# Kernel tuning notes

Hardware: AMD Instinct MI355X
Metric: run time of the kernel (lower is better)

## Reference

```python
import jax, jax.numpy as jnp
import numpy as np

D_MODEL = 512
NHEAD = 8
D_K = D_MODEL // NHEAD
SCALE = float(np.sqrt(D_K))


def setup_inputs() -> dict:
    key = jax.random.key(0)
    ks = jax.random.split(key, 11)
    B, S = 2, 4096
    std = 1.0 / np.sqrt(D_MODEL)
    inp = {
        'q': jax.random.normal(ks[0], (B, S, D_MODEL), jnp.float32),
        'k': jax.random.normal(ks[1], (B, S, D_MODEL), jnp.float32),
        'v': jax.random.normal(ks[2], (B, S, D_MODEL), jnp.float32),
        'w_q': jax.random.normal(ks[3], (D_MODEL, D_MODEL), jnp.float32) * std,
        'b_q': jax.random.normal(ks[4], (D_MODEL,), jnp.float32) * std,
        'w_k': jax.random.normal(ks[5], (D_MODEL, D_MODEL), jnp.float32) * std,
        'b_k': jax.random.normal(ks[6], (D_MODEL,), jnp.float32) * std,
        'w_v': jax.random.normal(ks[7], (D_MODEL, D_MODEL), jnp.float32) * std,
        'b_v': jax.random.normal(ks[8], (D_MODEL,), jnp.float32) * std,
        'w_o': jax.random.normal(ks[9], (D_MODEL, D_MODEL), jnp.float32) * std,
        'b_o': jax.random.normal(ks[10], (D_MODEL,), jnp.float32) * std,
    }
    return inp


def reference(q, k, v, w_q, b_q, w_k, b_k, w_v, b_v, w_o, b_o):
    B, S, _ = q.shape
    # torch Linear: y = x @ W.T + b
    def proj(x, W, b):
        y = x @ W.T + b
        return y.reshape(B, -1, NHEAD, D_K).transpose(0, 2, 1, 3)  # [B,H,S,Dk]
    qh = proj(q, w_q, b_q)
    kh = proj(k, w_k, b_k)
    vh = proj(v, w_v, b_v)
    scores = jnp.einsum('bhsd,bhtd->bhst', qh, kh) / SCALE  # [B,H,S,S]
    attn = jax.nn.softmax(scores, axis=-1)
    out = jnp.einsum('bhst,bhtd->bhsd', attn, vh)  # [B,H,S,Dk]
    out = out.transpose(0, 2, 1, 3).reshape(B, S, D_MODEL)
    return out @ w_o.T + b_o
```

## Files before the change

### kernel.cpp

```cpp
#include <hip/hip_runtime.h>
#include <stdint.h>

#define DM 512
#define S_LEN 4096
#define NH 8
#define DK 64

typedef __attribute__((ext_vector_type(8))) short bf16x8;
typedef __attribute__((ext_vector_type(4))) float f32x4;

#define QSCALE 0.18033688011112042f
#define NEGBIAS -17.312340490667562f

__device__ inline ushort f2bf(float f) {
  union { float f; uint32_t u; } v; v.f = f;
  uint32_t r = v.u + 0x7fff + ((v.u >> 16) & 1);
  return (ushort)(r >> 16);
}
__device__ inline uint32_t fu(float f) {
  union { float f; uint32_t u; } v; v.f = f; return v.u;
}
__device__ inline uint32_t pktrunc(float lo, float hi) {
  return __builtin_amdgcn_perm(fu(hi), fu(lo), 0x07060302);
}

__device__ inline void async_cp16(const ushort* g, ushort* l) {
  __builtin_amdgcn_global_load_lds((const __attribute__((address_space(1))) void*)g,
                                   (__attribute__((address_space(3))) void*)l, 16, 0, 0);
}

__global__ __launch_bounds__(256) void cvt_w(const float4* __restrict__ s0, ushort* __restrict__ d0,
                                             const float4* __restrict__ s1, ushort* __restrict__ d1,
                                             const float4* __restrict__ s2, ushort* __restrict__ d2,
                                             const float4* __restrict__ s3, ushort* __restrict__ d3) {
  int i = blockIdx.x * 256 + threadIdx.x;
  {
    float4 v = s0[i];
    ushort4 o = {f2bf(v.x), f2bf(v.y), f2bf(v.z), f2bf(v.w)};
    *(ushort4*)&d0[i * 4] = o;
  }
  {
    float4 v = s1[i];
    ushort4 o = {f2bf(v.x), f2bf(v.y), f2bf(v.z), f2bf(v.w)};
    *(ushort4*)&d1[i * 4] = o;
  }
  {
    float4 v = s2[i];
    ushort4 o = {f2bf(v.x), f2bf(v.y), f2bf(v.z), f2bf(v.w)};
    *(ushort4*)&d2[i * 4] = o;
  }
  {
    float4 v = s3[i];
    ushort4 o = {f2bf(v.x), f2bf(v.y), f2bf(v.z), f2bf(v.w)};
    *(ushort4*)&d3[i * 4] = o;
  }
}

__global__ __launch_bounds__(256) void gemm_proj(
    const float* __restrict__ q, const float* __restrict__ k, const float* __restrict__ v,
    const ushort* __restrict__ wq, const ushort* __restrict__ wk, const ushort* __restrict__ wv,
    const float* __restrict__ bq, const float* __restrict__ bk, const float* __restrict__ bv,
    ushort* __restrict__ Qh, ushort* __restrict__ Kh, ushort* __restrict__ VhT) {
  const float* A; const ushort* Bt; const float* bias; float cs;
  if (blockIdx.z == 0)      { A = q; Bt = wq; bias = bq; cs = QSCALE; }
  else if (blockIdx.z == 1) { A = k; Bt = wk; bias = bk; cs = 1.0f; }
  else                      { A = v; Bt = wv; bias = bv; cs = 1.0f; }

  __shared__ ushort As[64 * 32];
  __shared__ ushort Bs[128 * 32];
  const int tid = threadIdx.x;
  const int w = tid >> 6, lane = tid & 63;
  const int quad = lane >> 4, l16 = lane & 15;
  const int wm = w >> 1, wn = w & 1;
  const int m0 = blockIdx.y * 64, n0 = blockIdx.x * 128;
  const f32x4 zero4 = {0.f, 0.f, 0.f, 0.f};

  f32x4 acc[2][4];
  #pragma unroll
  for (int i = 0; i < 2; i++)
    #pragma unroll
    for (int j = 0; j < 4; j++) acc[i][j] = zero4;

  for (int kb = 0; kb < 16; kb++) {
    const int k0 = kb * 32;
    #pragma unroll
    for (int r = 0; r < 2; r++) {
      int idx = r * 256 + tid;
      async_cp16(&Bt[(size_t)(n0 + (idx >> 2)) * DM + k0 + (idx & 3) * 8], &Bs[idx * 8]);
    }
    {
      int row = tid >> 2, col = (tid & 3) * 8;
      const float* src = &A[(size_t)(m0 + row) * DM + k0 + col];
      float4 a0 = *(const float4*)src;
      float4 a1 = *(const float4*)(src + 4);
      uint2 w0 = {pktrunc(a0.x, a0.y), pktrunc(a0.z, a0.w)};
      uint2 w1 = {pktrunc(a1.x, a1.y), pktrunc(a1.z, a1.w)};
      *(uint2*)&As[row * 32 + col] = w0;
      *(uint2*)&As[row * 32 + col + 4] = w1;
    }
    __syncthreads();
    bf16x8 af[2], bfr[4];
    #pragma unroll
    for (int i = 0; i < 2; i++)
      af[i] = *(const bf16x8*)&As[(wm * 32 + i * 16 + l16) * 32 + quad * 8];
    #pragma unroll
    for (int j = 0; j < 4; j++)
      bfr[j] = *(const bf16x8*)&Bs[(wn * 64 + j * 16 + l16) * 32 + quad * 8];
    #pragma unroll
    for (int i = 0; i < 2; i++)
      #pragma unroll
      for (int j = 0; j < 4; j++)
        acc[i][j] = __builtin_amdgcn_mfma_f32_16x16x32_bf16(af[i], bfr[j], acc[i][j], 0, 0, 0);
    __syncthreads();
  }

  if (blockIdx.z != 2) {
    ushort* C = (blockIdx.z == 0) ? Qh : Kh;
    #pragma unroll
    for (int j = 0; j < 4; j++) {
      int col_g = n0 + wn * 64 + j * 16 + l16;
      float bv = bias[col_g];
      int h = col_g >> 6, d = col_g & 63;
      #pragma unroll
      for (int i = 0; i < 2; i++) {
        #pragma unroll
        for (int r = 0; r < 4; r++) {
          int row_g = m0 + wm * 32 + i * 16 + quad * 4 + r;
          int b = row_g >> 12, s = row_g & 4095;
          C[(((size_t)(b * NH + h) << 12) + s) * DK + d] = f2bf((acc[i][j][r] + bv) * cs);
        }
      }
    }
  } else {
    #pragma unroll
    for (int j = 0; j < 4; j++) {
      int col_g = n0 + wn * 64 + j * 16 + l16;
      float bv = bias[col_g];
      int h = col_g >> 6, d = col_g & 63;
      #pragma unroll
      for (int i = 0; i < 2; i++) {
        int row0 = m0 + wm * 32 + i * 16 + quad * 4;
        int b = row0 >> 12, s0 = row0 & 4095;
        ushort4 pk = {f2bf(acc[i][j][0] + bv), f2bf(acc[i][j][1] + bv),
                      f2bf(acc[i][j][2] + bv), f2bf(acc[i][j][3] + bv)};
        *(ushort4*)&VhT[((size_t)(b * NH + h) * DK + d) * S_LEN + s0] = pk;
      }
    }
  }
}

__global__ __launch_bounds__(256) void gemm_out(const ushort* __restrict__ A,
                                                const ushort* __restrict__ Bt,
                                                const float* __restrict__ bias,
                                                float* __restrict__ C) {
  __shared__ ushort As[64 * 32];
  __shared__ ushort Bs[128 * 32];
  const int tid = threadIdx.x;
  const int w = tid >> 6, lane = tid & 63;
  const int quad = lane >> 4, l16 = lane & 15;
  const int wm = w >> 1, wn = w & 1;
  const int m0 = blockIdx.y * 64, n0 = blockIdx.x * 128;
  const f32x4 zero4 = {0.f, 0.f, 0.f, 0.f};

  f32x4 acc[2][4];
  #pragma unroll
  for (int i = 0; i < 2; i++)
    #pragma unroll
    for (int j = 0; j < 4; j++) acc[i][j] = zero4;

  for (int kb = 0; kb < 16; kb++) {
    const int k0 = kb * 32;
    async_cp16(&A[(size_t)(m0 + (tid >> 2)) * DM + k0 + (tid & 3) * 8], &As[tid * 8]);
    #pragma unroll
    for (int r = 0; r < 2; r++) {
      int idx = r * 256 + tid;
      async_cp16(&Bt[(size_t)(n0 + (idx >> 2)) * DM + k0 + (idx & 3) * 8], &Bs[idx * 8]);
    }
    __syncthreads();
    bf16x8 af[2], bfr[4];
    #pragma unroll
    for (int i = 0; i < 2; i++)
      af[i] = *(const bf16x8*)&As[(wm * 32 + i * 16 + l16) * 32 + quad * 8];
    #pragma unroll
    for (int j = 0; j < 4; j++)
      bfr[j] = *(const bf16x8*)&Bs[(wn * 64 + j * 16 + l16) * 32 + quad * 8];
    #pragma unroll
    for (int i = 0; i < 2; i++)
      #pragma unroll
      for (int j = 0; j < 4; j++)
        acc[i][j] = __builtin_amdgcn_mfma_f32_16x16x32_bf16(af[i], bfr[j], acc[i][j], 0, 0, 0);
    __syncthreads();
  }

  #pragma unroll
  for (int j = 0; j < 4; j++) {
    int col_g = n0 + wn * 64 + j * 16 + l16;
    float bv = bias[col_g];
    #pragma unroll
    for (int i = 0; i < 2; i++) {
      #pragma unroll
      for (int r = 0; r < 4; r++) {
        int row_g = m0 + wm * 32 + i * 16 + quad * 4 + r;
        C[(size_t)row_g * DM + col_g] = acc[i][j][r] + bv;
      }
    }
  }
}

__global__ __launch_bounds__(256, 2) void attn(const ushort* __restrict__ Qh,
                                               const ushort* __restrict__ Kh,
                                               const ushort* __restrict__ VhT,
                                               ushort* __restrict__ O) {
  __shared__ ushort Ks[128 * 72];
  __shared__ ushort Vt[64 * 136];
  const int tid = threadIdx.x;
  const int w = tid >> 6, lane = tid & 63;
  const int quad = lane >> 4, l16 = lane & 15;
  const int bh = blockIdx.x;
  const int q0 = blockIdx.y * 128 + w * 32;
  const size_t base = (size_t)bh * S_LEN * DK;
  const f32x4 zero4 = {0.f, 0.f, 0.f, 0.f};
  const f32x4 negb = {NEGBIAS, NEGBIAS, NEGBIAS, NEGBIAS};
  const short one_bf = (short)0x3F80;
  const bf16x8 ones = {one_bf, one_bf, one_bf, one_bf, one_bf, one_bf, one_bf, one_bf};

  bf16x8 qf[2][2];
  #pragma unroll
  for (int i = 0; i < 2; i++)
    #pragma unroll
    for (int c = 0; c < 2; c++)
      qf[i][c] = *(const bf16x8*)&Qh[base + (size_t)(q0 + i * 16 + l16) * DK + c * 32 + quad * 8];

  f32x4 o[2][4];
  f32x4 l_acc[2];
  #pragma unroll
  for (int i = 0; i < 2; i++) {
    l_acc[i] = zero4;
    #pragma unroll
    for (int n = 0; n < 4; n++) o[i][n] = zero4;
  }

  for (int it = 0; it < 32; it++) {
    const int t0 = it * 128;
    #pragma unroll
    for (int r = 0; r < 4; r++) {
      int idx = r * 256 + tid;
      int row = idx >> 3, col = (idx & 7) * 8;
      *(uint4*)&Ks[row * 72 + col] = *(const uint4*)&Kh[base + (size_t)(t0 + row) * DK + col];
    }
    #pragma unroll
    for (int r = 0; r < 4; r++) {
      int idx = r * 256 + tid;
      int row = idx >> 4, colc = (idx & 15) * 8;
      uint4 vv = *(const uint4*)&VhT[base + (size_t)row * S_LEN + t0 + colc];
      int bpos = (colc & ~31) + ((colc >> 2) & 3) * 8 + ((colc >> 4) & 1) * 4;
      uint2 lo = {vv.x, vv.y}, hi = {vv.z, vv.w};
      *(uint2*)&Vt[row * 136 + bpos] = lo;
      *(uint2*)&Vt[row * 136 + bpos + 8] = hi;
    }
    __syncthreads();

    #pragma unroll
    for (int half = 0; half < 2; half++) {
      bf16x8 kf[4][2];
      #pragma unroll
      for (int s = 0; s < 4; s++) {
        int sub = half * 4 + s;
        kf[s][0] = *(const bf16x8*)&Ks[(sub * 16 + l16) * 72 + quad * 8];
        kf[s][1] = *(const bf16x8*)&Ks[(sub * 16 + l16) * 72 + 32 + quad * 8];
      }
      f32x4 sc[2][4];
      #pragma unroll
      for (int i = 0; i < 2; i++)
        #pragma unroll
        for (int s = 0; s < 4; s++) {
          f32x4 t = negb;
          t = __builtin_amdgcn_mfma_f32_16x16x32_bf16(kf[s][0], qf[i][0], t, 0, 0, 0);
          t = __builtin_amdgcn_mfma_f32_16x16x32_bf16(kf[s][1], qf[i][1], t, 0, 0, 0);
          sc[i][s] = t;
        }
      float p[2][4][4];
      #pragma unroll
      for (int i = 0; i < 2; i++)
        #pragma unroll
        for (int s = 0; s < 4; s++)
          #pragma unroll
          for (int r = 0; r < 4; r++)
            p[i][s][r] = __builtin_amdgcn_exp2f(sc[i][s][r]);
      union { bf16x8 v; uint32_t u[4]; } pf[2][2];
      #pragma unroll
      for (int i = 0; i < 2; i++)
        #pragma unroll
        for (int ppl = 0; ppl < 2; ppl++) {
          int s0 = ppl * 2, s1 = ppl * 2 + 1;
          pf[i][ppl].u[0] = pktrunc(p[i][s0][0], p[i][s0][1]);
          pf[i][ppl].u[1] = pktrunc(p[i][s0][2], p[i][s0][3]);
          pf[i][ppl].u[2] = pktrunc(p[i][s1][0], p[i][s1][1]);
          pf[i][ppl].u[3] = pktrunc(p[i][s1][2], p[i][s1][3]);
          l_acc[i] = __builtin_amdgcn_mfma_f32_16x16x32_bf16(pf[i][ppl].v, ones, l_acc[i], 0, 0, 0);
        }
      bf16x8 vf[4][2];
      #pragma unroll
      for (int n = 0; n < 4; n++)
        #pragma unroll
        for (int ppl = 0; ppl < 2; ppl++)
          vf[n][ppl] = *(const bf16x8*)&Vt[(n * 16 + l16) * 136 + (half * 2 + ppl) * 32 + quad * 8];
      #pragma unroll
      for (int n = 0; n < 4; n++)
        #pragma unroll
        for (int ppl = 0; ppl < 2; ppl++)
          #pragma unroll
          for (int i = 0; i < 2; i++)
            o[i][n] = __builtin_amdgcn_mfma_f32_16x16x32_bf16(pf[i][ppl].v, vf[n][ppl], o[i][n], 0, 0, 0);
    }
    __syncthreads();
  }

  const int b = bh >> 3, h = bh & 7;
  #pragma unroll
  for (int i = 0; i < 2; i++) {
    #pragma unroll
    for (int r = 0; r < 4; r++) {
      float inv = 1.0f / l_acc[i][r];
      int qq = q0 + i * 16 + quad * 4 + r;
      #pragma unroll
      for (int n = 0; n < 4; n++) {
        int d = n * 16 + l16;
        O[(size_t)(b * S_LEN + qq) * DM + h * DK + d] = f2bf(o[i][n][r] * inv);
      }
    }
  }
}

extern "C" void kernel_launch(void* const* d_in, const int* in_sizes, int n_in,
                              void* d_out, int out_size, void* d_ws, size_t ws_size,
                              hipStream_t stream) {
  const float* q   = (const float*)d_in[0];
  const float* k   = (const float*)d_in[1];
  const float* v   = (const float*)d_in[2];
  const float* w_q = (const float*)d_in[3];
  const float* b_q = (const float*)d_in[4];
  const float* w_k = (const float*)d_in[5];
  const float* b_k = (const float*)d_in[6];
  const float* w_v = (const float*)d_in[7];
  const float* b_v = (const float*)d_in[8];
  const float* w_o = (const float*)d_in[9];
  const float* b_o = (const float*)d_in[10];

  const size_t W_ELEMS = (size_t)DM * DM;
  const size_t HEADS_ELEMS = (size_t)2 * NH * S_LEN * DK;
  ushort* wqb = (ushort*)d_ws;
  ushort* wkb = wqb + W_ELEMS;
  ushort* wvb = wkb + W_ELEMS;
  ushort* wob = wvb + W_ELEMS;
  ushort* Qh  = wob + W_ELEMS;
  ushort* Kh  = Qh + HEADS_ELEMS;
  ushort* VhT = Kh + HEADS_ELEMS;
  ushort* AttO = VhT + HEADS_ELEMS;

  cvt_w<<<256, 256, 0, stream>>>((const float4*)w_q, wqb, (const float4*)w_k, wkb,
                                 (const float4*)w_v, wvb, (const float4*)w_o, wob);
  gemm_proj<<<dim3(4, 128, 3), 256, 0, stream>>>(q, k, v, wqb, wkb, wvb,
                                                 b_q, b_k, b_v, Qh, Kh, VhT);
  attn<<<dim3(16, 32), 256, 0, stream>>>(Qh, Kh, VhT, AttO);
  gemm_out<<<dim3(4, 128), 256, 0, stream>>>(AttO, wob, b_o, (float*)d_out);
}
```

Baseline: 233.9 us.

## Load GEMM fragments directly from global memory, removing LDS staging and barriers

Both projection GEMMs now have each lane load its MFMA operand fragments straight from global memory into registers. This removes the shared-memory tiles, the async global-to-LDS copies and the two barriers per k-step, and unrolls the k loop by two. Each weight and activation fragment is now fetched by several waves instead of once per block, so more global/L2 traffic and less coalesced row-strided access are traded for no synchronization.

```diff
diff --git a/kernel.cpp b/kernel.cpp
--- a/kernel.cpp
+++ b/kernel.cpp
@@ -22,11 +22,6 @@
 }
 __device__ inline uint32_t pktrunc(float lo, float hi) {
   return __builtin_amdgcn_perm(fu(hi), fu(lo), 0x07060302);
-}
-
-__device__ inline void async_cp16(const ushort* g, ushort* l) {
-  __builtin_amdgcn_global_load_lds((const __attribute__((address_space(1))) void*)g,
-                                   (__attribute__((address_space(3))) void*)l, 16, 0, 0);
 }
 
 __global__ __launch_bounds__(256) void cvt_w(const float4* __restrict__ s0, ushort* __restrict__ d0,
@@ -66,8 +61,6 @@
   else if (blockIdx.z == 1) { A = k; Bt = wk; bias = bk; cs = 1.0f; }
   else                      { A = v; Bt = wv; bias = bv; cs = 1.0f; }
 
-  __shared__ ushort As[64 * 32];
-  __shared__ ushort Bs[128 * 32];
   const int tid = threadIdx.x;
   const int w = tid >> 6, lane = tid & 63;
   const int quad = lane >> 4, l16 = lane & 15;
@@ -81,37 +74,33 @@
     #pragma unroll
     for (int j = 0; j < 4; j++) acc[i][j] = zero4;
 
+  const float* Ar0 = &A[(size_t)(m0 + wm * 32 + l16) * DM + quad * 8];
+  const float* Ar1 = Ar0 + (size_t)16 * DM;
+  const ushort* Br[4];
+  #pragma unroll
+  for (int j = 0; j < 4; j++)
+    Br[j] = &Bt[(size_t)(n0 + wn * 64 + j * 16 + l16) * DM + quad * 8];
+
+  #pragma unroll 2
   for (int kb = 0; kb < 16; kb++) {
     const int k0 = kb * 32;
-    #pragma unroll
-    for (int r = 0; r < 2; r++) {
-      int idx = r * 256 + tid;
-      async_cp16(&Bt[(size_t)(n0 + (idx >> 2)) * DM + k0 + (idx & 3) * 8], &Bs[idx * 8]);
-    }
-    {
-      int row = tid >> 2, col = (tid & 3) * 8;
-      const float* src = &A[(size_t)(m0 + row) * DM + k0 + col];
-      float4 a0 = *(const float4*)src;
-      float4 a1 = *(const float4*)(src + 4);
-      uint2 w0 = {pktrunc(a0.x, a0.y), pktrunc(a0.z, a0.w)};
-      uint2 w1 = {pktrunc(a1.x, a1.y), pktrunc(a1.z, a1.w)};
-      *(uint2*)&As[row * 32 + col] = w0;
-      *(uint2*)&As[row * 32 + col + 4] = w1;
-    }
-    __syncthreads();
-    bf16x8 af[2], bfr[4];
-    #pragma unroll
-    for (int i = 0; i < 2; i++)
-      af[i] = *(const bf16x8*)&As[(wm * 32 + i * 16 + l16) * 32 + quad * 8];
-    #pragma unroll
-    for (int j = 0; j < 4; j++)
-      bfr[j] = *(const bf16x8*)&Bs[(wn * 64 + j * 16 + l16) * 32 + quad * 8];
-    #pragma unroll
-    for (int i = 0; i < 2; i++)
-      #pragma unroll
-      for (int j = 0; j < 4; j++)
-        acc[i][j] = __builtin_amdgcn_mfma_f32_16x16x32_bf16(af[i], bfr[j], acc[i][j], 0, 0, 0);
-    __syncthreads();
+    float4 a00 = *(const float4*)&Ar0[k0];
+    float4 a01 = *(const float4*)&Ar0[k0 + 4];
+    float4 a10 = *(const float4*)&Ar1[k0];
+    float4 a11 = *(const float4*)&Ar1[k0 + 4];
+    bf16x8 bfr[4];
+    #pragma unroll
+    for (int j = 0; j < 4; j++) bfr[j] = *(const bf16x8*)&Br[j][k0];
+    union { bf16x8 v; uint32_t u[4]; } af0, af1;
+    af0.u[0] = pktrunc(a00.x, a00.y); af0.u[1] = pktrunc(a00.z, a00.w);
+    af0.u[2] = pktrunc(a01.x, a01.y); af0.u[3] = pktrunc(a01.z, a01.w);
+    af1.u[0] = pktrunc(a10.x, a10.y); af1.u[1] = pktrunc(a10.z, a10.w);
+    af1.u[2] = pktrunc(a11.x, a11.y); af1.u[3] = pktrunc(a11.z, a11.w);
+    #pragma unroll
+    for (int j = 0; j < 4; j++) {
+      acc[0][j] = __builtin_amdgcn_mfma_f32_16x16x32_bf16(af0.v, bfr[j], acc[0][j], 0, 0, 0);
+      acc[1][j] = __builtin_amdgcn_mfma_f32_16x16x32_bf16(af1.v, bfr[j], acc[1][j], 0, 0, 0);
+    }
   }
 
   if (blockIdx.z != 2) {
@@ -153,8 +142,6 @@
                                                 const ushort* __restrict__ Bt,
                                                 const float* __restrict__ bias,
                                                 float* __restrict__ C) {
-  __shared__ ushort As[64 * 32];
-  __shared__ ushort Bs[128 * 32];
   const int tid = threadIdx.x;
   const int w = tid >> 6, lane = tid & 63;
   const int quad = lane >> 4, l16 = lane & 15;
@@ -168,28 +155,26 @@
     #pragma unroll
     for (int j = 0; j < 4; j++) acc[i][j] = zero4;
 
+  const ushort* Ar0 = &A[(size_t)(m0 + wm * 32 + l16) * DM + quad * 8];
+  const ushort* Ar1 = Ar0 + (size_t)16 * DM;
+  const ushort* Br[4];
+  #pragma unroll
+  for (int j = 0; j < 4; j++)
+    Br[j] = &Bt[(size_t)(n0 + wn * 64 + j * 16 + l16) * DM + quad * 8];
+
+  #pragma unroll 2
   for (int kb = 0; kb < 16; kb++) {
     const int k0 = kb * 32;
-    async_cp16(&A[(size_t)(m0 + (tid >> 2)) * DM + k0 + (tid & 3) * 8], &As[tid * 8]);
-    #pragma unroll
-    for (int r = 0; r < 2; r++) {
-      int idx = r * 256 + tid;
-      async_cp16(&Bt[(size_t)(n0 + (idx >> 2)) * DM + k0 + (idx & 3) * 8], &Bs[idx * 8]);
-    }
-    __syncthreads();
-    bf16x8 af[2], bfr[4];
-    #pragma unroll
-    for (int i = 0; i < 2; i++)
-      af[i] = *(const bf16x8*)&As[(wm * 32 + i * 16 + l16) * 32 + quad * 8];
-    #pragma unroll
-    for (int j = 0; j < 4; j++)
-      bfr[j] = *(const bf16x8*)&Bs[(wn * 64 + j * 16 + l16) * 32 + quad * 8];
-    #pragma unroll
-    for (int i = 0; i < 2; i++)
-      #pragma unroll
-      for (int j = 0; j < 4; j++)
-        acc[i][j] = __builtin_amdgcn_mfma_f32_16x16x32_bf16(af[i], bfr[j], acc[i][j], 0, 0, 0);
-    __syncthreads();
+    bf16x8 af0 = *(const bf16x8*)&Ar0[k0];
+    bf16x8 af1 = *(const bf16x8*)&Ar1[k0];
+    bf16x8 bfr[4];
+    #pragma unroll
+    for (int j = 0; j < 4; j++) bfr[j] = *(const bf16x8*)&Br[j][k0];
+    #pragma unroll
+    for (int j = 0; j < 4; j++) {
+      acc[0][j] = __builtin_amdgcn_mfma_f32_16x16x32_bf16(af0, bfr[j], acc[0][j], 0, 0, 0);
+      acc[1][j] = __builtin_amdgcn_mfma_f32_16x16x32_bf16(af1, bfr[j], acc[1][j], 0, 0, 0);
+    }
   }
 
   #pragma unroll
```

Result: slower. 289.6 us (+23.8%).
